# Performance work log

Hardware: AMD Instinct MI355X
Metric: run time of the kernel (lower is better)

Reference implementation:

```python
import jax, jax.numpy as jnp
import numpy as np

N, F, V, E = 16384, 39, 100000, 16
H1, H2 = 400, 400
EPS = 1e-5

def setup_inputs() -> dict:
    key = jax.random.key(0)
    ks = jax.random.split(key, 12)
    xi = jax.random.randint(ks[0], (N, F, 1), 0, V)  # indices per field
    xv = jax.random.uniform(ks[1], (N, F), dtype=jnp.float32)
    # stacked per-field embedding tables (each table has V+1 rows)
    emb1 = jax.random.normal(ks[2], (F, V + 1), dtype=jnp.float32)          # 1st-order
    emb2 = jax.random.normal(ks[3], (F, V + 1, E), dtype=jnp.float32)       # 2nd-order
    D = F * E
    W1 = jax.random.normal(ks[4], (D, H1), dtype=jnp.float32) / np.sqrt(D)
    b1 = jnp.zeros((H1,), jnp.float32)
    g1 = jnp.ones((H1,), jnp.float32)
    be1 = jnp.zeros((H1,), jnp.float32)
    W2 = jax.random.normal(ks[5], (H1, H2), dtype=jnp.float32) / np.sqrt(H1)
    b2 = jnp.zeros((H2,), jnp.float32)
    g2 = jnp.ones((H2,), jnp.float32)
    be2 = jnp.zeros((H2,), jnp.float32)
    bias = jax.random.normal(ks[6], (1,), dtype=jnp.float32)
    return dict(xi=xi, xv=xv, emb1=emb1, emb2=emb2, W1=W1, b1=b1, g1=g1, be1=be1,
                W2=W2, b2=b2, g2=g2, be2=be2, bias=bias)

def _batchnorm(x, g, b):
    # BatchNorm1d in training mode: batch mean/var (biased)
    mu = x.mean(0)
    var = x.var(0)
    return g * (x - mu) * jax.lax.rsqrt(var + EPS) + b

def reference(xi, xv, emb1, emb2, W1, b1, g1, be1, W2, b2, g2, be2, bias):
    idx = xi[:, :, 0]                     # (N, F)
    f_ids = jnp.arange(F)[None, :]        # (1, F)
    e1 = emb1[f_ids, idx] * xv            # (N, F): per-field 1st-order term
    e2 = emb2[f_ids, idx] * xv[:, :, None]  # (N, F, E)
    s = e2.sum(axis=1)                    # (N, E) sum of embeddings
    fm2 = 0.5 * (s * s - (e2 * e2).sum(axis=1))  # (N, E) FM 2nd-order
    deep = e2.reshape(e2.shape[0], F * E)
    h = _batchnorm(deep @ W1 + b1, g1, be1)       # dropout = identity (eval)
    h = _batchnorm(h @ W2 + b2, g2, be2)
    return e1.sum(axis=1) + fm2.sum(axis=1) + h.sum(axis=1) + bias[0]
```

## Files before the change

### kernel.cpp

```cpp
#include <hip/hip_runtime.h>
#include <hip/hip_bf16.h>

#define Nn 16384
#define Ff 39
#define Vv 100000
#define Ee 16
#define Dd 624
#define KP1 640
#define KP2 448
#define Hh 400
#define EPSf 1e-5f

typedef short short8 __attribute__((ext_vector_type(8)));
typedef float floatx4 __attribute__((ext_vector_type(4)));

__device__ __forceinline__ unsigned short f2bu(float x) {
  __hip_bfloat16 h = __float2bfloat16(x);
  return *reinterpret_cast<unsigned short*>(&h);
}
__device__ __forceinline__ float bf2f(unsigned short v) {
  union { unsigned int u; float f; } x; x.u = ((unsigned int)v) << 16; return x.f;
}

__device__ __forceinline__ void gload16(void* lds, const void* g) {
  __builtin_amdgcn_global_load_lds(
      (const __attribute__((address_space(1))) unsigned int*)g,
      (__attribute__((address_space(3))) unsigned int*)lds, 16, 0, 0);
}

__global__ __launch_bounds__(256) void embed_kernel(
    const int* __restrict__ xi, const float* __restrict__ xv,
    const float* __restrict__ emb1, const float* __restrict__ emb2,
    const float* __restrict__ bias, const float* __restrict__ W1,
    __hip_bfloat16* __restrict__ deep, float* __restrict__ p,
    __hip_bfloat16* __restrict__ W1t, float* __restrict__ stats,
    __hip_bfloat16* __restrict__ x1b) {
  const int b = blockIdx.x;
  if (b >= 4096) {
    if (b == 4496) {
      for (int i = threadIdx.x; i < 1600; i += 256) stats[i] = 0.f;
    } else {
      const int n = b - 4096;
      for (int k = threadIdx.x; k < KP1; k += 256)
        W1t[(size_t)n * KP1 + k] =
            (k < Dd) ? __float2bfloat16(W1[(size_t)k * Hh + n]) : __float2bfloat16(0.f);
    }
    return;
  }
  __shared__ int   sidx[4][40];
  __shared__ float sxv[4][40];
  const int w = threadIdx.x >> 6;
  const int lane = threadIdx.x & 63;
  const int n = b * 4 + w;
  if (lane < Ff) {
    sidx[w][lane] = xi[n * Ff + lane];
    sxv[w][lane]  = xv[n * Ff + lane];
  }
  __syncthreads();

  const float4* e2v = (const float4*)emb2;
  float se0 = 0.f, se1 = 0.f, se2 = 0.f, se3 = 0.f;
  float qe0 = 0.f, qe1 = 0.f, qe2 = 0.f, qe3 = 0.f;
  #pragma unroll
  for (int t = 0; t < 3; ++t) {
    const int j4 = lane + t * 64;
    if (j4 < 156) {
      const int f = j4 >> 2;
      float4 v = e2v[((long)f * (Vv + 1) + sidx[w][f]) * 4 + (j4 & 3)];
      const float xf = sxv[w][f];
      v.x *= xf; v.y *= xf; v.z *= xf; v.w *= xf;
      *(ushort4*)&deep[(size_t)n * KP1 + j4 * 4] =
          make_ushort4(f2bu(v.x), f2bu(v.y), f2bu(v.z), f2bu(v.w));
      se0 += v.x; qe0 += v.x * v.x;
      se1 += v.y; qe1 += v.y * v.y;
      se2 += v.z; qe2 += v.z * v.z;
      se3 += v.w; qe3 += v.w * v.w;
    }
  }
  if (lane < 4)  *(ushort4*)&deep[(size_t)n * KP1 + Dd + lane * 4] = make_ushort4(0, 0, 0, 0);
  if (lane < 12) *(ushort4*)&x1b [(size_t)n * KP2 + Hh + lane * 4] = make_ushort4(0, 0, 0, 0);

  #pragma unroll
  for (int d = 4; d < 64; d <<= 1) {
    se0 += __shfl_xor(se0, d); qe0 += __shfl_xor(qe0, d);
    se1 += __shfl_xor(se1, d); qe1 += __shfl_xor(qe1, d);
    se2 += __shfl_xor(se2, d); qe2 += __shfl_xor(qe2, d);
    se3 += __shfl_xor(se3, d); qe3 += __shfl_xor(qe3, d);
  }
  float val = 0.f;
  if (lane < 4)
    val = 0.5f * ((se0 * se0 - qe0) + (se1 * se1 - qe1) +
                  (se2 * se2 - qe2) + (se3 * se3 - qe3));
  if (lane < Ff)
    val += emb1[(long)lane * (Vv + 1) + sidx[w][lane]] * sxv[w][lane];
  #pragma unroll
  for (int d = 1; d < 64; d <<= 1) val += __shfl_xor(val, d);
  if (lane == 0) p[n] = val + bias[0];
}

__global__ __launch_bounds__(256) void gemm_bf16(
    const __hip_bfloat16* __restrict__ A, const __hip_bfloat16* __restrict__ Wt,
    const float* __restrict__ bias, __hip_bfloat16* __restrict__ C,
    float* __restrict__ s, float* __restrict__ ss, const int K, const int ldc) {
  __shared__ __align__(16) short As_s[128 * 64];
  __shared__ __align__(16) short Bs_s[80 * 64];
  __shared__ float redS[4][5][16], redQ[4][5][16];
  const int tid = threadIdx.x;
  const int lin = blockIdx.x + blockIdx.y * 5;
  const int v   = (lin & 7) * 80 + (lin >> 3);
  const int n0  = (v % 5) * 80;
  const int m0  = (v / 5) * 128;
  const int w = tid >> 6, lane = tid & 63;
  const int lm = lane & 15, qd = lane >> 4;

  floatx4 acc[2][5];
  #pragma unroll
  for (int i = 0; i < 2; ++i)
    #pragma unroll
    for (int j = 0; j < 5; ++j)
      acc[i][j] = (floatx4){0.f, 0.f, 0.f, 0.f};

  const int nk = K >> 6;
  for (int ks = 0; ks < nk; ++ks) {
    const int k0 = ks << 6;
    #pragma unroll
    for (int j = 0; j < 4; ++j) {
      const int c = tid + j * 256;
      const int m = c >> 3, kc = c & 7;
      gload16(&As_s[c * 8], &A[(size_t)(m0 + m) * K + k0 + ((kc ^ (m & 7)) << 3)]);
    }
    #pragma unroll
    for (int j = 0; j < 3; ++j) {
      const int c = tid + j * 256;
      if (c < 640) {
        const int nn = c >> 3, kc = c & 7;
        gload16(&Bs_s[c * 8], &Wt[(size_t)(n0 + nn) * K + k0 + ((kc ^ (nn & 7)) << 3)]);
      }
    }
    __syncthreads();
    #pragma unroll
    for (int h = 0; h < 2; ++h) {
      const int sl = (h * 32 + qd * 8) >> 3;
      const int r0 = w * 32 + lm, r1 = r0 + 16;
      const short8 a0 = *(const short8*)&As_s[r0 * 64 + ((sl ^ (r0 & 7)) << 3)];
      const short8 a1 = *(const short8*)&As_s[r1 * 64 + ((sl ^ (r1 & 7)) << 3)];
      #pragma unroll
      for (int nt = 0; nt < 5; ++nt) {
        const int rn = nt * 16 + lm;
        const short8 bfr = *(const short8*)&Bs_s[rn * 64 + ((sl ^ (rn & 7)) << 3)];
        acc[0][nt] = __builtin_amdgcn_mfma_f32_16x16x32_bf16(a0, bfr, acc[0][nt], 0, 0, 0);
        acc[1][nt] = __builtin_amdgcn_mfma_f32_16x16x32_bf16(a1, bfr, acc[1][nt], 0, 0, 0);
      }
    }
    __syncthreads();
  }

  const int rb = m0 + w * 32 + qd * 4;
  #pragma unroll
  for (int nt = 0; nt < 5; ++nt) {
    const int col = n0 + nt * 16 + lm;
    const float bc = bias[col];
    float cs = 0.f, cq = 0.f;
    #pragma unroll
    for (int mt = 0; mt < 2; ++mt) {
      #pragma unroll
      for (int r = 0; r < 4; ++r) {
        const float vv = acc[mt][nt][r] + bc;
        const __hip_bfloat16 hv = __float2bfloat16(vv);
        C[(size_t)(rb + mt * 16 + r) * ldc + col] = hv;
        const float vf = __bfloat162float(hv);
        cs += vf; cq += vf * vf;
      }
    }
    cs += __shfl_xor(cs, 16); cq += __shfl_xor(cq, 16);
    cs += __shfl_xor(cs, 32); cq += __shfl_xor(cq, 32);
    if (lane < 16) { redS[w][nt][lm] = cs; redQ[w][nt][lm] = cq; }
  }
  __syncthreads();
  if (tid < 80) {
    const int nt = tid >> 4, l = tid & 15;
    const int col = n0 + nt * 16 + l;
    atomicAdd(&s[col],  redS[0][nt][l] + redS[1][nt][l] + redS[2][nt][l] + redS[3][nt][l]);
    atomicAdd(&ss[col], redQ[0][nt][l] + redQ[1][nt][l] + redQ[2][nt][l] + redQ[3][nt][l]);
  }
}

__global__ __launch_bounds__(256) void prep2_kernel(
    const float* __restrict__ W2,
    const float* __restrict__ s1, const float* __restrict__ ss1,
    const float* __restrict__ g1, const float* __restrict__ be1,
    const float* __restrict__ b2, __hip_bfloat16* __restrict__ W2t, float* __restrict__ b2p) {
  __shared__ float sa1[Hh], sc1[Hh];
  __shared__ float red[256];
  const int n = blockIdx.x, t = threadIdx.x;
  for (int k = t; k < Hh; k += 256) {
    const float mu = s1[k] * (1.f / Nn);
    const float var = ss1[k] * (1.f / Nn) - mu * mu;
    const float a = g1[k] * rsqrtf(var + EPSf);
    sa1[k] = a;
    sc1[k] = be1[k] - a * mu;
  }
  __syncthreads();
  float acc = 0.f;
  for (int k = t; k < KP2; k += 256) {
    if (k < Hh) {
      const float wv = W2[(size_t)k * Hh + n];
      W2t[(size_t)n * KP2 + k] = __float2bfloat16(sa1[k] * wv);
      acc += sc1[k] * wv;
    } else {
      W2t[(size_t)n * KP2 + k] = __float2bfloat16(0.f);
    }
  }
  red[t] = acc; __syncthreads();
  for (int d = 128; d > 0; d >>= 1) { if (t < d) red[t] += red[t + d]; __syncthreads(); }
  if (t == 0) b2p[n] = b2[n] + red[0];
}

__global__ __launch_bounds__(256) void final_kernel(
    const __hip_bfloat16* __restrict__ x2,
    const float* __restrict__ s2, const float* __restrict__ ss2,
    const float* __restrict__ g2, const float* __restrict__ be2,
    const float* __restrict__ p, float* __restrict__ out) {
  __shared__ float sal[Hh];
  __shared__ float red[256];
  const int t = threadIdx.x;
  float part = 0.f;
  for (int h = t; h < Hh; h += 256) {
    const float mu = s2[h] * (1.f / Nn);
    const float var = ss2[h] * (1.f / Nn) - mu * mu;
    const float al = g2[h] * rsqrtf(var + EPSf);
    sal[h] = al;
    part += be2[h] - al * mu;
  }
  red[t] = part; __syncthreads();
  for (int d = 128; d > 0; d >>= 1) { if (t < d) red[t] += red[t + d]; __syncthreads(); }
  __syncthreads();
  const float c2 = red[0];

  const int w = t >> 6, lane = t & 63;
  const int n = blockIdx.x * 4 + w;
  const unsigned short* row = (const unsigned short*)(x2 + (size_t)n * Hh);
  float acc = 0.f;
  for (int h0 = lane * 4; h0 < Hh; h0 += 256) {
    const ushort4 u = *(const ushort4*)&row[h0];
    acc += bf2f(u.x) * sal[h0] + bf2f(u.y) * sal[h0 + 1]
         + bf2f(u.z) * sal[h0 + 2] + bf2f(u.w) * sal[h0 + 3];
  }
  #pragma unroll
  for (int d = 1; d < 64; d <<= 1) acc += __shfl_xor(acc, d);
  if (lane == 0) out[n] = p[n] + acc + c2;
}

extern "C" void kernel_launch(void* const* d_in, const int* in_sizes, int n_in,
                              void* d_out, int out_size, void* d_ws, size_t ws_size,
                              hipStream_t stream) {
  const int*   xi   = (const int*)d_in[0];
  const float* xv   = (const float*)d_in[1];
  const float* emb1 = (const float*)d_in[2];
  const float* emb2 = (const float*)d_in[3];
  const float* W1   = (const float*)d_in[4];
  const float* b1   = (const float*)d_in[5];
  const float* g1   = (const float*)d_in[6];
  const float* be1  = (const float*)d_in[7];
  const float* W2   = (const float*)d_in[8];
  const float* b2   = (const float*)d_in[9];
  const float* g2   = (const float*)d_in[10];
  const float* be2  = (const float*)d_in[11];
  const float* bias = (const float*)d_in[12];
  float* out = (float*)d_out;

  char* ws = (char*)d_ws;
  __hip_bfloat16* deep = (__hip_bfloat16*)ws;  ws += (size_t)Nn * KP1 * 2;
  __hip_bfloat16* x1b  = (__hip_bfloat16*)ws;  ws += (size_t)Nn * KP2 * 2;
  __hip_bfloat16* x2b  = (__hip_bfloat16*)ws;  ws += (size_t)Nn * Hh * 2;
  __hip_bfloat16* W1t  = (__hip_bfloat16*)ws;  ws += (size_t)Hh * KP1 * 2;
  __hip_bfloat16* W2t  = (__hip_bfloat16*)ws;  ws += (size_t)Hh * KP2 * 2;
  float* p    = (float*)ws;  ws += (size_t)Nn * 4;
  float* s1   = (float*)ws;  ws += Hh * 4;
  float* ss1  = (float*)ws;  ws += Hh * 4;
  float* s2   = (float*)ws;  ws += Hh * 4;
  float* ss2  = (float*)ws;  ws += Hh * 4;
  float* b2p  = (float*)ws;  ws += Hh * 4;

  embed_kernel<<<4497, 256, 0, stream>>>(xi, xv, emb1, emb2, bias, W1, deep, p, W1t, s1, x1b);
  gemm_bf16<<<dim3(5, Nn / 128), 256, 0, stream>>>(deep, W1t, b1, x1b, s1, ss1, KP1, KP2);
  prep2_kernel<<<Hh, 256, 0, stream>>>(W2, s1, ss1, g1, be1, b2, W2t, b2p);
  gemm_bf16<<<dim3(5, Nn / 128), 256, 0, stream>>>(x1b, W2t, b2p, x2b, s2, ss2, KP2, Hh);
  final_kernel<<<Nn / 4, 256, 0, stream>>>(x2b, s2, ss2, g2, be2, p, out);
}
```

Before: 381.1 us.

## Skip storing second GEMM output; fold BN2 and row-sum into projection vector

The second GEMM now only accumulates the column sum and sum of squares for BN2 and no longer writes x2 to memory. Because the final output only needs the row sum of the BN2 output, a new prep3 kernel folds the BN2 scale and W2t into a vector u and a constant. The final kernel then takes a dot product of x1 with u. The W1 and W2 transposes now use 64x64 LDS-tiled blocks with coalesced writes, b2p is accumulated with atomics, and the emb1 load in the embed kernel is issued earlier. This drops a 13 MB write and its read-back, in exchange for statistics computed on unrounded fp32 values and a small extra kernel launch.

```diff
diff --git a/kernel.cpp b/kernel.cpp
--- a/kernel.cpp
+++ b/kernel.cpp
@@ -36,27 +36,49 @@
     __hip_bfloat16* __restrict__ W1t, float* __restrict__ stats,
     __hip_bfloat16* __restrict__ x1b) {
   const int b = blockIdx.x;
-  if (b >= 4096) {
-    if (b == 4496) {
-      for (int i = threadIdx.x; i < 1600; i += 256) stats[i] = 0.f;
-    } else {
-      const int n = b - 4096;
-      for (int k = threadIdx.x; k < KP1; k += 256)
-        W1t[(size_t)n * KP1 + k] =
-            (k < Dd) ? __float2bfloat16(W1[(size_t)k * Hh + n]) : __float2bfloat16(0.f);
-    }
-    return;
-  }
+  __shared__ float Tt[64][65];
   __shared__ int   sidx[4][40];
   __shared__ float sxv[4][40];
+  if (b < 70) {
+    const int tk = b / 7, tn = b % 7;
+    const int k0 = tk * 64, n0 = tn * 64;
+    const int c = threadIdx.x & 63, r0 = (threadIdx.x >> 6) * 16;
+    const int n = n0 + c;
+    #pragma unroll
+    for (int r = r0; r < r0 + 16; ++r) {
+      const int k = k0 + r;
+      Tt[c][r] = (k < Dd && n < Hh) ? W1[(size_t)k * Hh + n] : 0.f;
+    }
+    __syncthreads();
+    const int nl = threadIdx.x >> 2, kq = (threadIdx.x & 3) * 16;
+    const int nw = n0 + nl;
+    if (nw < Hh) {
+      #pragma unroll
+      for (int q = 0; q < 4; ++q) {
+        const int kk = kq + q * 4;
+        *(ushort4*)&W1t[(size_t)nw * KP1 + k0 + kk] = make_ushort4(
+            f2bu(Tt[nl][kk]), f2bu(Tt[nl][kk + 1]),
+            f2bu(Tt[nl][kk + 2]), f2bu(Tt[nl][kk + 3]));
+      }
+    }
+    return;
+  }
+  if (b == 70) {
+    for (int i = threadIdx.x; i < 2000; i += 256) stats[i] = 0.f;
+    return;
+  }
   const int w = threadIdx.x >> 6;
   const int lane = threadIdx.x & 63;
-  const int n = b * 4 + w;
+  const int n = (b - 71) * 4 + w;
   if (lane < Ff) {
     sidx[w][lane] = xi[n * Ff + lane];
     sxv[w][lane]  = xv[n * Ff + lane];
   }
   __syncthreads();
+
+  float e1v = 0.f;
+  if (lane < Ff)
+    e1v = emb1[(long)lane * (Vv + 1) + sidx[w][lane]] * sxv[w][lane];
 
   const float4* e2v = (const float4*)emb2;
   float se0 = 0.f, se1 = 0.f, se2 = 0.f, se3 = 0.f;
@@ -91,8 +113,7 @@
   if (lane < 4)
     val = 0.5f * ((se0 * se0 - qe0) + (se1 * se1 - qe1) +
                   (se2 * se2 - qe2) + (se3 * se3 - qe3));
-  if (lane < Ff)
-    val += emb1[(long)lane * (Vv + 1) + sidx[w][lane]] * sxv[w][lane];
+  val += e1v;
   #pragma unroll
   for (int d = 1; d < 64; d <<= 1) val += __shfl_xor(val, d);
   if (lane == 0) p[n] = val + bias[0];
@@ -166,9 +187,12 @@
       #pragma unroll
       for (int r = 0; r < 4; ++r) {
         const float vv = acc[mt][nt][r] + bc;
-        const __hip_bfloat16 hv = __float2bfloat16(vv);
-        C[(size_t)(rb + mt * 16 + r) * ldc + col] = hv;
-        const float vf = __bfloat162float(hv);
+        float vf = vv;
+        if (C) {
+          const __hip_bfloat16 hv = __float2bfloat16(vv);
+          C[(size_t)(rb + mt * 16 + r) * ldc + col] = hv;
+          vf = __bfloat162float(hv);
+        }
         cs += vf; cq += vf * vf;
       }
     }
@@ -190,65 +214,111 @@
     const float* __restrict__ s1, const float* __restrict__ ss1,
     const float* __restrict__ g1, const float* __restrict__ be1,
     const float* __restrict__ b2, __hip_bfloat16* __restrict__ W2t, float* __restrict__ b2p) {
-  __shared__ float sa1[Hh], sc1[Hh];
-  __shared__ float red[256];
-  const int n = blockIdx.x, t = threadIdx.x;
-  for (int k = t; k < Hh; k += 256) {
-    const float mu = s1[k] * (1.f / Nn);
-    const float var = ss1[k] * (1.f / Nn) - mu * mu;
-    const float a = g1[k] * rsqrtf(var + EPSf);
-    sa1[k] = a;
-    sc1[k] = be1[k] - a * mu;
-  }
-  __syncthreads();
-  float acc = 0.f;
-  for (int k = t; k < KP2; k += 256) {
+  __shared__ float sa[64], sc[64];
+  __shared__ float Tt[64][65];
+  __shared__ float pcs[256];
+  const int tb = blockIdx.x;
+  const int tk = tb / 7, tn = tb % 7;
+  const int k0 = tk * 64, n0 = tn * 64;
+  const int t = threadIdx.x;
+  if (t < 64) {
+    const int k = k0 + t;
+    float a = 0.f, cv = 0.f;
     if (k < Hh) {
-      const float wv = W2[(size_t)k * Hh + n];
-      W2t[(size_t)n * KP2 + k] = __float2bfloat16(sa1[k] * wv);
-      acc += sc1[k] * wv;
-    } else {
-      W2t[(size_t)n * KP2 + k] = __float2bfloat16(0.f);
-    }
-  }
-  red[t] = acc; __syncthreads();
-  for (int d = 128; d > 0; d >>= 1) { if (t < d) red[t] += red[t + d]; __syncthreads(); }
-  if (t == 0) b2p[n] = b2[n] + red[0];
-}
-
-__global__ __launch_bounds__(256) void final_kernel(
-    const __hip_bfloat16* __restrict__ x2,
+      const float mu = s1[k] * (1.f / Nn);
+      const float var = ss1[k] * (1.f / Nn) - mu * mu;
+      a = g1[k] * rsqrtf(var + EPSf);
+      cv = be1[k] - a * mu;
+    }
+    sa[t] = a; sc[t] = cv;
+  }
+  __syncthreads();
+  const int c = t & 63, r0 = (t >> 6) * 16;
+  const int n = n0 + c;
+  float pc = 0.f;
+  #pragma unroll
+  for (int r = r0; r < r0 + 16; ++r) {
+    const int k = k0 + r;
+    const float wv = (k < Hh && n < Hh) ? W2[(size_t)k * Hh + n] : 0.f;
+    Tt[c][r] = sa[r] * wv;
+    pc += sc[r] * wv;
+  }
+  pcs[t] = pc;
+  __syncthreads();
+  if (t < 64 && n0 + t < Hh) {
+    float tot = pcs[t] + pcs[t + 64] + pcs[t + 128] + pcs[t + 192];
+    if (k0 == 0) tot += b2[n0 + t];
+    atomicAdd(&b2p[n0 + t], tot);
+  }
+  const int nl = t >> 2, kq = (t & 3) * 16;
+  const int nw = n0 + nl;
+  if (nw < Hh) {
+    #pragma unroll
+    for (int q = 0; q < 4; ++q) {
+      const int kk = kq + q * 4;
+      *(ushort4*)&W2t[(size_t)nw * KP2 + k0 + kk] = make_ushort4(
+          f2bu(Tt[nl][kk]), f2bu(Tt[nl][kk + 1]),
+          f2bu(Tt[nl][kk + 2]), f2bu(Tt[nl][kk + 3]));
+    }
+  }
+}
+
+__global__ __launch_bounds__(256) void prep3_kernel(
+    const __hip_bfloat16* __restrict__ W2t,
     const float* __restrict__ s2, const float* __restrict__ ss2,
     const float* __restrict__ g2, const float* __restrict__ be2,
-    const float* __restrict__ p, float* __restrict__ out) {
+    const float* __restrict__ b2p, float* __restrict__ u) {
   __shared__ float sal[Hh];
+  __shared__ float part[4][64];
   __shared__ float red[256];
   const int t = threadIdx.x;
-  float part = 0.f;
+  float cpart = 0.f;
   for (int h = t; h < Hh; h += 256) {
     const float mu = s2[h] * (1.f / Nn);
     const float var = ss2[h] * (1.f / Nn) - mu * mu;
     const float al = g2[h] * rsqrtf(var + EPSf);
     sal[h] = al;
-    part += be2[h] - al * mu;
-  }
-  red[t] = part; __syncthreads();
-  for (int d = 128; d > 0; d >>= 1) { if (t < d) red[t] += red[t + d]; __syncthreads(); }
-  __syncthreads();
-  const float c2 = red[0];
-
+    cpart += be2[h] - al * mu + al * b2p[h];
+  }
+  __syncthreads();
+  const int k = blockIdx.x * 64 + (t & 63);
+  const int hs = t >> 6;
+  float acc = 0.f;
+  for (int h = hs * 100; h < hs * 100 + 100; ++h)
+    acc += sal[h] * bf2f(*(const unsigned short*)&W2t[(size_t)h * KP2 + k]);
+  part[hs][t & 63] = acc;
+  __syncthreads();
+  if (t < 64) u[blockIdx.x * 64 + t] = part[0][t] + part[1][t] + part[2][t] + part[3][t];
+  if (blockIdx.x == 0) {
+    red[t] = cpart;
+    __syncthreads();
+    for (int d = 128; d > 0; d >>= 1) { if (t < d) red[t] += red[t + d]; __syncthreads(); }
+    if (t == 0) u[KP2] = red[0];
+  }
+}
+
+__global__ __launch_bounds__(256) void final_kernel(
+    const __hip_bfloat16* __restrict__ x1, const float* __restrict__ u,
+    const float* __restrict__ p, float* __restrict__ out) {
+  __shared__ float su[KP2];
+  __shared__ float scc;
+  const int t = threadIdx.x;
+  for (int i = t; i < KP2; i += 256) su[i] = u[i];
+  if (t == 0) scc = u[KP2];
+  __syncthreads();
   const int w = t >> 6, lane = t & 63;
   const int n = blockIdx.x * 4 + w;
-  const unsigned short* row = (const unsigned short*)(x2 + (size_t)n * Hh);
+  const unsigned short* row = (const unsigned short*)(x1 + (size_t)n * KP2);
   float acc = 0.f;
-  for (int h0 = lane * 4; h0 < Hh; h0 += 256) {
-    const ushort4 u = *(const ushort4*)&row[h0];
-    acc += bf2f(u.x) * sal[h0] + bf2f(u.y) * sal[h0 + 1]
-         + bf2f(u.z) * sal[h0 + 2] + bf2f(u.w) * sal[h0 + 3];
+  #pragma unroll
+  for (int h0 = lane * 4; h0 < KP2; h0 += 256) {
+    const ushort4 uv = *(const ushort4*)&row[h0];
+    acc += bf2f(uv.x) * su[h0]     + bf2f(uv.y) * su[h0 + 1]
+         + bf2f(uv.z) * su[h0 + 2] + bf2f(uv.w) * su[h0 + 3];
   }
   #pragma unroll
   for (int d = 1; d < 64; d <<= 1) acc += __shfl_xor(acc, d);
-  if (lane == 0) out[n] = p[n] + acc + c2;
+  if (lane == 0) out[n] = p[n] + acc + scc;
 }
 
 extern "C" void kernel_launch(void* const* d_in, const int* in_sizes, int n_in,
@@ -272,7 +342,6 @@
   char* ws = (char*)d_ws;
   __hip_bfloat16* deep = (__hip_bfloat16*)ws;  ws += (size_t)Nn * KP1 * 2;
   __hip_bfloat16* x1b  = (__hip_bfloat16*)ws;  ws += (size_t)Nn * KP2 * 2;
-  __hip_bfloat16* x2b  = (__hip_bfloat16*)ws;  ws += (size_t)Nn * Hh * 2;
   __hip_bfloat16* W1t  = (__hip_bfloat16*)ws;  ws += (size_t)Hh * KP1 * 2;
   __hip_bfloat16* W2t  = (__hip_bfloat16*)ws;  ws += (size_t)Hh * KP2 * 2;
   float* p    = (float*)ws;  ws += (size_t)Nn * 4;
@@ -281,10 +350,12 @@
   float* s2   = (float*)ws;  ws += Hh * 4;
   float* ss2  = (float*)ws;  ws += Hh * 4;
   float* b2p  = (float*)ws;  ws += Hh * 4;
-
-  embed_kernel<<<4497, 256, 0, stream>>>(xi, xv, emb1, emb2, bias, W1, deep, p, W1t, s1, x1b);
+  float* u    = (float*)ws;  ws += (KP2 + 1) * 4;
+
+  embed_kernel<<<4167, 256, 0, stream>>>(xi, xv, emb1, emb2, bias, W1, deep, p, W1t, s1, x1b);
   gemm_bf16<<<dim3(5, Nn / 128), 256, 0, stream>>>(deep, W1t, b1, x1b, s1, ss1, KP1, KP2);
-  prep2_kernel<<<Hh, 256, 0, stream>>>(W2, s1, ss1, g1, be1, b2, W2t, b2p);
-  gemm_bf16<<<dim3(5, Nn / 128), 256, 0, stream>>>(x1b, W2t, b2p, x2b, s2, ss2, KP2, Hh);
-  final_kernel<<<Nn / 4, 256, 0, stream>>>(x2b, s2, ss2, g2, be2, p, out);
-}
+  prep2_kernel<<<49, 256, 0, stream>>>(W2, s1, ss1, g1, be1, b2, W2t, b2p);
+  gemm_bf16<<<dim3(5, Nn / 128), 256, 0, stream>>>(x1b, W2t, b2p, nullptr, s2, ss2, KP2, 0);
+  prep3_kernel<<<7, 256, 0, stream>>>(W2t, s2, ss2, g2, be2, b2p, u);
+  final_kernel<<<Nn / 4, 256, 0, stream>>>(x1b, u, p, out);
+}
```

Result: no change. 387.7 us (+1.7%).
